# Kernel optimization log

Measured on AMD Instinct MI355X. Metric: run time of the kernel, lower is better.

## Reference

```python
import jax, jax.numpy as jnp
import numpy as np

DIM = 2048
HEADS = 16
B = 2
T = 2048


def setup_inputs() -> dict:
    key = jax.random.key(0)
    k_x, k_qkv, k_out, k_b = jax.random.split(key, 4)
    inv = DIM ** -0.5
    return {
        "x": jax.random.normal(k_x, (B, T, DIM), dtype=jnp.float32),
        "w_qkv": jax.random.normal(k_qkv, (DIM, 3 * DIM), dtype=jnp.float32) * inv,
        "w_out": jax.random.normal(k_out, (DIM, DIM), dtype=jnp.float32) * inv,
        "b_out": jnp.zeros((DIM,), dtype=jnp.float32),
    }


def reference(x, w_qkv, w_out, b_out):
    b, t, e = x.shape
    h = HEADS
    d = e // h
    scale = d ** -0.5
    qkv = x @ w_qkv                              # [b, t, 3e]
    q, k, v = jnp.split(qkv, 3, axis=-1)
    # [b, t, e] -> [b, h, t, d]
    q, k, v = (a.reshape(b, t, h, d).transpose(0, 2, 1, 3) for a in (q, k, v))
    dots = jnp.einsum("bhid,bhjd->bhij", q, k) * scale  # [b, h, t, t]
    causal_mask = jnp.triu(jnp.ones((t, t), dtype=bool), k=1)  # True where j > i
    dots = jnp.where(causal_mask[None, None, :, :], -jnp.inf, dots)
    attn = jax.nn.softmax(dots, axis=-1)
    out = jnp.einsum("bhij,bhjd->bhid", attn, v)  # [b, h, t, d]
    out = out.transpose(0, 2, 1, 3).reshape(b, t, e)
    return out @ w_out + b_out
```

## Files before the change

### kernel.cpp

```cpp
#include <hip/hip_runtime.h>
#include <stdint.h>

#define BATCH 2
#define TDIM 2048
#define EDIM 2048
#define NH 16
#define HD 128
#define E3 6144
#define MROWS 4096

typedef short v8bf __attribute__((ext_vector_type(8)));
typedef float v4f  __attribute__((ext_vector_type(4)));

typedef __attribute__((address_space(3))) uint8_t lds_u8;
typedef __attribute__((address_space(1))) uint8_t glb_u8;

__device__ __forceinline__ void gload16(const void* g, void* l) {
    __builtin_amdgcn_global_load_lds((const glb_u8*)g, (lds_u8*)l, 16, 0, 0);
}

__device__ __forceinline__ ushort f2bf(float f) {
    uint32_t u = __float_as_uint(f);
    return (ushort)((u + 0x7fffu + ((u >> 16) & 1u)) >> 16);
}

__global__ void cvtx_kernel(const float* __restrict__ in, ushort* __restrict__ out, int n) {
    int i = (blockIdx.x * 256 + threadIdx.x) * 4;
    const int stride = gridDim.x * 256 * 4;
    for (; i < n; i += stride) {
        const float4 v = *reinterpret_cast<const float4*>(in + i);
        ushort4 o = make_ushort4(f2bf(v.x), f2bf(v.y), f2bf(v.z), f2bf(v.w));
        *reinterpret_cast<ushort4*>(out + i) = o;
    }
}

__global__ void tcvt_kernel(const float* __restrict__ in, ushort* __restrict__ out, int R, int C) {
    __shared__ float t[32][33];
    const int tc = blockIdx.x * 32;
    const int tr = blockIdx.y * 32;
    const int tid = threadIdx.x;
    const int row = tid >> 3, c4 = (tid & 7) * 4;
    const float4 v = *reinterpret_cast<const float4*>(in + (size_t)(tr + row) * C + tc + c4);
    t[row][c4] = v.x; t[row][c4 + 1] = v.y; t[row][c4 + 2] = v.z; t[row][c4 + 3] = v.w;
    __syncthreads();
    const int oc = tid >> 3, r4 = (tid & 7) * 4;
    ushort4 o = make_ushort4(f2bf(t[r4][oc]), f2bf(t[r4 + 1][oc]),
                             f2bf(t[r4 + 2][oc]), f2bf(t[r4 + 3][oc]));
    *reinterpret_cast<ushort4*>(out + (size_t)(tc + oc) * R + tr + r4) = o;
}

__global__ void vtrans_kernel(const ushort* __restrict__ qkv, ushort* __restrict__ vt) {
    __shared__ ushort t[32][33];
    const int bh = blockIdx.z;
    const int b = bh >> 4, h = bh & 15;
    const int tr = blockIdx.x * 32;
    const int tc = blockIdx.y * 32;
    const int tid = threadIdx.x;
    const int row = tid >> 3, c4 = (tid & 7) * 4;
    const ushort4 v = *reinterpret_cast<const ushort4*>(
        qkv + (size_t)(b * TDIM + tr + row) * E3 + 2 * EDIM + h * HD + tc + c4);
    t[row][c4] = v.x; t[row][c4 + 1] = v.y; t[row][c4 + 2] = v.z; t[row][c4 + 3] = v.w;
    __syncthreads();
    const int oc = tid >> 3, r4 = (tid & 7) * 4;
    ushort4 o = make_ushort4(t[r4][oc], t[r4 + 1][oc], t[r4 + 2][oc], t[r4 + 3][oc]);
    *reinterpret_cast<ushort4*>(vt + (size_t)(bh * HD + tc + oc) * TDIM + tr + r4) = o;
}

__global__ __launch_bounds__(512, 2) void gemm256_kernel(const ushort* __restrict__ A,
                                                         const ushort* __restrict__ Bt,
                                                         ushort* __restrict__ C,
                                                         int Mdim, int Ndim, int Kdim) {
    __shared__ __align__(16) ushort Al[2][256 * 64];
    __shared__ __align__(16) ushort Bl[2][256 * 64];
    const int tid = threadIdx.x;
    const int lane = tid & 63;
    const int wv = tid >> 6;
    const int l4 = lane >> 4, l16 = lane & 15;
    const int wr = wv >> 2, wc = wv & 3;
    const int nbn = Ndim >> 8;
    const int nwg = (Mdim >> 8) * nbn;
    int bid = blockIdx.x;
    bid = (bid & 7) * (nwg >> 3) + (bid >> 3);
    const int bm = bid / nbn, bn = bid % nbn;

    const ushort* Abase = A + (size_t)(bm * 256) * Kdim;
    const ushort* Bbase = Bt + (size_t)(bn * 256) * Kdim;
    const int NT = Kdim >> 6;

    v4f acc[8][4] = {};

#define STAGE256(BUF, KT)                                                                     \
    do {                                                                                      \
        _Pragma("unroll") for (int i = 0; i < 4; ++i) {                                       \
            const int c = i * 512 + tid;                                                      \
            const int row = c >> 3;                                                           \
            const int kc = (c & 7) ^ (row & 7);                                               \
            gload16(Abase + (size_t)row * Kdim + (KT) * 64 + kc * 8,                          \
                    &Al[BUF][(i * 512 + wv * 64) * 8]);                                       \
        }                                                                                     \
        _Pragma("unroll") for (int i = 0; i < 4; ++i) {                                       \
            const int c = i * 512 + tid;                                                      \
            const int row = c >> 3;                                                           \
            const int kc = (c & 7) ^ (row & 7);                                               \
            gload16(Bbase + (size_t)row * Kdim + (KT) * 64 + kc * 8,                          \
                    &Bl[BUF][(i * 512 + wv * 64) * 8]);                                       \
        }                                                                                     \
    } while (0)

    STAGE256(0, 0);
    STAGE256(1, 1);
    asm volatile("s_waitcnt vmcnt(8)" ::: "memory");
    __builtin_amdgcn_s_barrier();
    asm volatile("" ::: "memory");

    int cur = 0;
    for (int t = 0; t < NT; ++t) {
        const ushort* As = &Al[cur][0];
        const ushort* Bs = &Bl[cur][0];
#pragma unroll
        for (int mh = 0; mh < 2; ++mh) {
            v8bf af[4][2];
#pragma unroll
            for (int m = 0; m < 4; ++m)
#pragma unroll
                for (int kk = 0; kk < 2; ++kk) {
                    const int r = wr * 128 + mh * 64 + m * 16 + l16;
                    const int slot = (kk * 4 + l4) ^ (l16 & 7);
                    af[m][kk] = *reinterpret_cast<const v8bf*>(&As[r * 64 + slot * 8]);
                }
#pragma unroll
            for (int nh = 0; nh < 2; ++nh) {
                v8bf bfr[2][2];
#pragma unroll
                for (int n = 0; n < 2; ++n)
#pragma unroll
                    for (int kk = 0; kk < 2; ++kk) {
                        const int r = wc * 64 + nh * 32 + n * 16 + l16;
                        const int slot = (kk * 4 + l4) ^ (l16 & 7);
                        bfr[n][kk] = *reinterpret_cast<const v8bf*>(&Bs[r * 64 + slot * 8]);
                    }
                __builtin_amdgcn_s_setprio(1);
#pragma unroll
                for (int kk = 0; kk < 2; ++kk)
#pragma unroll
                    for (int m = 0; m < 4; ++m)
#pragma unroll
                        for (int n = 0; n < 2; ++n)
                            acc[mh * 4 + m][nh * 2 + n] = __builtin_amdgcn_mfma_f32_16x16x32_bf16(
                                af[m][kk], bfr[n][kk], acc[mh * 4 + m][nh * 2 + n], 0, 0, 0);
                __builtin_amdgcn_s_setprio(0);
            }
        }
        if (t == NT - 1) break;

        __builtin_amdgcn_sched_barrier(0);
        __builtin_amdgcn_s_barrier();
        asm volatile("" ::: "memory");
        if (t + 2 < NT) {
            STAGE256(cur, t + 2);
            asm volatile("s_waitcnt vmcnt(8)" ::: "memory");
        } else {
            asm volatile("s_waitcnt vmcnt(0)" ::: "memory");
        }
        __builtin_amdgcn_s_barrier();
        asm volatile("" ::: "memory");
        __builtin_amdgcn_sched_barrier(0);
        cur ^= 1;
    }
#undef STAGE256

    const int r0 = bm * 256 + wr * 128 + l4 * 4;
    const int c0 = bn * 256 + wc * 64 + l16;
#pragma unroll
    for (int mi = 0; mi < 8; ++mi)
#pragma unroll
        for (int ni = 0; ni < 4; ++ni)
#pragma unroll
            for (int j = 0; j < 4; ++j)
                C[(size_t)(r0 + mi * 16 + j) * Ndim + c0 + ni * 16] = f2bf(acc[mi][ni][j]);
}

template <int OUTF32>
__global__ void gemm_kernel(const ushort* __restrict__ A, const ushort* __restrict__ Bt,
                            void* __restrict__ Cv, const float* __restrict__ bias,
                            int Mdim, int Ndim, int Kdim) {
    __shared__ __align__(16) ushort As[128 * 64];
    __shared__ __align__(16) ushort Bs[128 * 64];
    const int tid = threadIdx.x;
    const int lane = tid & 63;
    const int wv = tid >> 6;
    const int l4 = lane >> 4, l16 = lane & 15;
    const int nbn = Ndim >> 7;
    const int nwg = (Mdim >> 7) * nbn;
    int bid = blockIdx.x;
    bid = (bid & 7) * (nwg >> 3) + (bid >> 3);
    const int bm = bid / nbn, bn = bid % nbn;
    const int wr = wv >> 1, wc = wv & 1;

    const ushort* Abase = A + (size_t)(bm * 128) * Kdim;
    const ushort* Bbase = Bt + (size_t)(bn * 128) * Kdim;

    v4f acc[4][4] = {};

    for (int k0 = 0; k0 < Kdim; k0 += 64) {
#pragma unroll
        for (int i = 0; i < 4; ++i) {
            const int c = i * 256 + tid;
            const int row = c >> 3;
            const int kc = (c & 7) ^ (row & 7);
            gload16(Abase + (size_t)row * Kdim + k0 + kc * 8, &As[(i * 256 + wv * 64) * 8]);
        }
#pragma unroll
        for (int i = 0; i < 4; ++i) {
            const int c = i * 256 + tid;
            const int row = c >> 3;
            const int kc = (c & 7) ^ (row & 7);
            gload16(Bbase + (size_t)row * Kdim + k0 + kc * 8, &Bs[(i * 256 + wv * 64) * 8]);
        }
        __syncthreads();
#pragma unroll
        for (int kk = 0; kk < 2; ++kk) {
            v8bf af[4], bfr[4];
#pragma unroll
            for (int m = 0; m < 4; ++m) {
                const int r = wr * 64 + m * 16 + l16;
                const int slot = (kk * 4 + l4) ^ (r & 7);
                af[m] = *reinterpret_cast<const v8bf*>(&As[r * 64 + slot * 8]);
            }
#pragma unroll
            for (int n = 0; n < 4; ++n) {
                const int r = wc * 64 + n * 16 + l16;
                const int slot = (kk * 4 + l4) ^ (r & 7);
                bfr[n] = *reinterpret_cast<const v8bf*>(&Bs[r * 64 + slot * 8]);
            }
#pragma unroll
            for (int m = 0; m < 4; ++m)
#pragma unroll
                for (int n = 0; n < 4; ++n)
                    acc[m][n] = __builtin_amdgcn_mfma_f32_16x16x32_bf16(af[m], bfr[n], acc[m][n], 0, 0, 0);
        }
        __syncthreads();
    }

    const int r0 = bm * 128 + wr * 64 + l4 * 4;
    const int c0 = bn * 128 + wc * 64 + l16;
    if (OUTF32) {
        float* Cf = (float*)Cv;
#pragma unroll
        for (int n = 0; n < 4; ++n) {
            const float bv = bias[c0 + n * 16];
#pragma unroll
            for (int m = 0; m < 4; ++m)
#pragma unroll
                for (int j = 0; j < 4; ++j)
                    Cf[(size_t)(r0 + m * 16 + j) * Ndim + c0 + n * 16] = acc[m][n][j] + bv;
        }
    } else {
        ushort* Cb = (ushort*)Cv;
#pragma unroll
        for (int n = 0; n < 4; ++n)
#pragma unroll
            for (int m = 0; m < 4; ++m)
#pragma unroll
                for (int j = 0; j < 4; ++j)
                    Cb[(size_t)(r0 + m * 16 + j) * Ndim + c0 + n * 16] = f2bf(acc[m][n][j]);
    }
}

__global__ __launch_bounds__(256, 2) void flash_kernel(const ushort* __restrict__ qkv,
                                                       const ushort* __restrict__ vt,
                                                       ushort* __restrict__ ao) {
    __shared__ __align__(16) ushort Kl[2][64 * 128];
    __shared__ __align__(16) ushort Vl[2][128 * 64];
    __shared__ __align__(16) ushort Pl[128 * 64];

    const int xi = blockIdx.x;
    const int ti = (xi & 1) ? (xi >> 1) : (15 - (xi >> 1));
    const int h = blockIdx.y;
    const int b = blockIdx.z;
    const int tid = threadIdx.x;
    const int lane = tid & 63;
    const int wv = tid >> 6;
    const int l4 = lane >> 4, l16 = lane & 15;

    const int rbs[2]  = {ti * 64 + wv * 16, TDIM - 64 * (ti + 1) + wv * 16};
    const int diag[2] = {ti, 31 - ti};
    const int nkt = 32 - ti;

    v8bf qf[2][4];
#pragma unroll
    for (int mg = 0; mg < 2; ++mg) {
        const ushort* qp = qkv + (size_t)(b * TDIM + rbs[mg] + l16) * E3 + h * HD + l4 * 8;
#pragma unroll
        for (int d0 = 0; d0 < 4; ++d0) {
            v8bf r = *reinterpret_cast<const v8bf*>(qp + d0 * 32);
            v8bf o;
#pragma unroll
            for (int e = 0; e < 8; ++e) {
                const float f = __uint_as_float(((uint32_t)(ushort)r[e]) << 16) * 0.08838834764831845f;
                o[e] = (short)f2bf(f);
            }
            qf[mg][d0] = o;
        }
    }

    float mrun[2][4], lrun[2][4];
#pragma unroll
    for (int mg = 0; mg < 2; ++mg)
#pragma unroll
        for (int j = 0; j < 4; ++j) { mrun[mg][j] = -1e30f; lrun[mg][j] = 0.0f; }
    v4f oacc[2][8] = {};

    const ushort* kbase = qkv + (size_t)(b * TDIM) * E3 + EDIM + h * HD;
    const ushort* vbase = vt + (size_t)((b * 16 + h) * HD) * TDIM;

#define STAGE(BUF, KT)                                                                        \
    do {                                                                                      \
        _Pragma("unroll") for (int i = 0; i < 4; ++i) {                                       \
            const int c = i * 256 + tid;                                                      \
            const int row = c >> 4;                                                           \
            const int dc = (c & 15) ^ (row & 7);                                              \
            gload16(kbase + (size_t)((KT) * 64 + row) * E3 + dc * 8,                          \
                    &Kl[BUF][(i * 256 + wv * 64) * 8]);                                       \
        }                                                                                     \
        _Pragma("unroll") for (int i = 0; i < 4; ++i) {                                       \
            const int c = i * 256 + tid;                                                      \
            const int row = c >> 3;                                                           \
            const int jc = (c & 7) ^ (row & 7);                                               \
            gload16(vbase + (size_t)row * TDIM + (KT) * 64 + jc * 8,                          \
                    &Vl[BUF][(i * 256 + wv * 64) * 8]);                                       \
        }                                                                                     \
    } while (0)

    STAGE(0, 0);
    __syncthreads();
    int cur = 0;

    for (int kt = 0; kt < nkt; ++kt) {
        if (kt + 1 < nkt) STAGE(cur ^ 1, kt + 1);

        const bool act0 = (kt <= diag[0]);
        const ushort* Kb = &Kl[cur][0];
        const ushort* Vb = &Vl[cur][0];

        v4f s[2][4] = {};
#pragma unroll
        for (int d0 = 0; d0 < 4; ++d0) {
            v8bf kf[4];
#pragma unroll
            for (int kvn = 0; kvn < 4; ++kvn) {
                const int r = kvn * 16 + l16;
                const int slot = (d0 * 4 + l4) ^ (r & 7);
                kf[kvn] = *reinterpret_cast<const v8bf*>(&Kb[r * 128 + slot * 8]);
            }
#pragma unroll
            for (int kvn = 0; kvn < 4; ++kvn) {
                if (act0)
                    s[0][kvn] = __builtin_amdgcn_mfma_f32_16x16x32_bf16(qf[0][d0], kf[kvn], s[0][kvn], 0, 0, 0);
                s[1][kvn] = __builtin_amdgcn_mfma_f32_16x16x32_bf16(qf[1][d0], kf[kvn], s[1][kvn], 0, 0, 0);
            }
        }

#pragma unroll
        for (int mg = 0; mg < 2; ++mg) {
            if (mg == 0 && !act0) continue;

            float sv[4][4];
#pragma unroll
            for (int kvn = 0; kvn < 4; ++kvn)
#pragma unroll
                for (int j = 0; j < 4; ++j)
                    sv[kvn][j] = s[mg][kvn][j];

            if (kt == diag[mg]) {
                const int rg = rbs[mg] + l4 * 4;
#pragma unroll
                for (int kvn = 0; kvn < 4; ++kvn) {
                    const int cg = kt * 64 + kvn * 16 + l16;
#pragma unroll
                    for (int j = 0; j < 4; ++j)
                        if (cg > rg + j) sv[kvn][j] = -__builtin_inff();
                }
            }

            float pm[4], dmax = -1e30f;
#pragma unroll
            for (int j = 0; j < 4; ++j) {
                float m0 = fmaxf(fmaxf(sv[0][j], sv[1][j]), fmaxf(sv[2][j], sv[3][j]));
                m0 = fmaxf(m0, __shfl_xor(m0, 1));
                m0 = fmaxf(m0, __shfl_xor(m0, 2));
                m0 = fmaxf(m0, __shfl_xor(m0, 4));
                m0 = fmaxf(m0, __shfl_xor(m0, 8));
                pm[j] = m0;
                dmax = fmaxf(dmax, m0 - mrun[mg][j]);
            }
            if (!__all(dmax <= 8.0f)) {
                float corr[4];
#pragma unroll
                for (int j = 0; j < 4; ++j) {
                    const float mn = fmaxf(mrun[mg][j], pm[j]);
                    corr[j] = __expf(mrun[mg][j] - mn);
                    mrun[mg][j] = mn;
                    lrun[mg][j] *= corr[j];
                }
#pragma unroll
                for (int n = 0; n < 8; ++n)
#pragma unroll
                    for (int j = 0; j < 4; ++j)
                        oacc[mg][n][j] *= corr[j];
            }

            float p[4][4];
#pragma unroll
            for (int kvn = 0; kvn < 4; ++kvn)
#pragma unroll
                for (int j = 0; j < 4; ++j)
                    p[kvn][j] = __expf(sv[kvn][j] - mrun[mg][j]);
#pragma unroll
            for (int j = 0; j < 4; ++j)
                lrun[mg][j] += p[0][j] + p[1][j] + p[2][j] + p[3][j];

            const int row = wv * 32 + mg * 16 + l4 * 4;
#pragma unroll
            for (int kvn = 0; kvn < 4; ++kvn) {
                const int cc = kvn * 2 + (l16 >> 3);
#pragma unroll
                for (int j = 0; j < 4; ++j) {
                    const int r = row + j;
                    Pl[r * 64 + ((cc ^ (r & 7)) * 8) + (l16 & 7)] = f2bf(p[kvn][j]);
                }
            }
        }

#pragma unroll
        for (int kk = 0; kk < 2; ++kk) {
            v8bf pf[2];
#pragma unroll
            for (int mg = 0; mg < 2; ++mg) {
                if (mg == 0 && !act0) continue;
                const int r = wv * 32 + mg * 16 + l16;
                const int slot = (kk * 4 + l4) ^ (r & 7);
                pf[mg] = *reinterpret_cast<const v8bf*>(&Pl[r * 64 + slot * 8]);
            }
#pragma unroll
            for (int n = 0; n < 8; ++n) {
                const int dr = n * 16 + l16;
                const int slot = (kk * 4 + l4) ^ (dr & 7);
                v8bf vf = *reinterpret_cast<const v8bf*>(&Vb[dr * 64 + slot * 8]);
                if (act0)
                    oacc[0][n] = __builtin_amdgcn_mfma_f32_16x16x32_bf16(pf[0], vf, oacc[0][n], 0, 0, 0);
                oacc[1][n] = __builtin_amdgcn_mfma_f32_16x16x32_bf16(pf[1], vf, oacc[1][n], 0, 0, 0);
            }
        }
        __syncthreads();
        cur ^= 1;
    }
#undef STAGE

#pragma unroll
    for (int mg = 0; mg < 2; ++mg) {
        float inv[4];
#pragma unroll
        for (int j = 0; j < 4; ++j) {
            float l = lrun[mg][j];
            l += __shfl_xor(l, 1);
            l += __shfl_xor(l, 2);
            l += __shfl_xor(l, 4);
            l += __shfl_xor(l, 8);
            inv[j] = 1.0f / l;
        }
        ushort* aop = ao + (size_t)(b * TDIM + rbs[mg] + l4 * 4) * EDIM + h * HD + l16;
#pragma unroll
        for (int n = 0; n < 8; ++n)
#pragma unroll
            for (int j = 0; j < 4; ++j)
                aop[(size_t)j * EDIM + n * 16] = f2bf(oacc[mg][n][j] * inv[j]);
    }
}

extern "C" void kernel_launch(void* const* d_in, const int* in_sizes, int n_in,
                              void* d_out, int out_size, void* d_ws, size_t ws_size,
                              hipStream_t stream) {
    (void)in_sizes; (void)n_in; (void)out_size; (void)ws_size;
    const float* x     = (const float*)d_in[0];
    const float* w_qkv = (const float*)d_in[1];
    const float* w_out = (const float*)d_in[2];
    const float* b_out = (const float*)d_in[3];

    uint8_t* ws = (uint8_t*)d_ws;
    ushort* qkv   = (ushort*)(ws);
    ushort* woutT = (ushort*)(ws + 50331648u);
    ushort* xb    = (ushort*)(ws + 58720256u);
    ushort* wqkvT = (ushort*)(ws + 75497472u);
    ushort* vtb   = xb;
    ushort* ao    = wqkvT;

    cvtx_kernel<<<2048, 256, 0, stream>>>(x, xb, MROWS * EDIM);
    tcvt_kernel<<<dim3(E3 / 32, EDIM / 32), 256, 0, stream>>>(w_qkv, wqkvT, EDIM, E3);
    tcvt_kernel<<<dim3(EDIM / 32, EDIM / 32), 256, 0, stream>>>(w_out, woutT, EDIM, EDIM);

    gemm256_kernel<<<(MROWS / 256) * (E3 / 256), 512, 0, stream>>>(
        xb, wqkvT, qkv, MROWS, E3, EDIM);

    vtrans_kernel<<<dim3(TDIM / 32, HD / 32, BATCH * NH), 256, 0, stream>>>(qkv, vtb);

    flash_kernel<<<dim3(16, NH, BATCH), 256, 0, stream>>>(qkv, vtb, ao);

    gemm_kernel<1><<<(MROWS / 128) * (EDIM / 128), 256, 0, stream>>>(
        ao, woutT, d_out, b_out, MROWS, EDIM, EDIM);
}
```

Measured before the change: 289.0 us.

## Restructure QKV GEMM into 128x256 tiles with split-phase staged loads

Replaces the 256x256-tile QKV projection GEMM with a 128x256-tile kernel. Each K step is split into two halves, and global-to-LDS loads for upcoming tiles are interleaved between the MFMA phases behind extra barriers. The aim is to overlap memory traffic with compute more finely, cut LDS and register footprint per block, and double the number of workgroups for better CU occupancy. In exchange, each block reuses its B tile over fewer rows, and each K step carries more barriers.

Result: faster. 276.7 us (-4.3%).

```diff
diff --git a/kernel.cpp b/kernel.cpp
--- a/kernel.cpp
+++ b/kernel.cpp
@@ -66,118 +66,137 @@
     *reinterpret_cast<ushort4*>(vt + (size_t)(bh * HD + tc + oc) * TDIM + tr + r4) = o;
 }
 
-__global__ __launch_bounds__(512, 2) void gemm256_kernel(const ushort* __restrict__ A,
-                                                         const ushort* __restrict__ Bt,
-                                                         ushort* __restrict__ C,
-                                                         int Mdim, int Ndim, int Kdim) {
-    __shared__ __align__(16) ushort Al[2][256 * 64];
-    __shared__ __align__(16) ushort Bl[2][256 * 64];
+__global__ __launch_bounds__(512, 2) void gemm8p_kernel(const ushort* __restrict__ A,
+                                                        const ushort* __restrict__ Bt,
+                                                        ushort* __restrict__ C,
+                                                        int Mdim, int Ndim, int Kdim) {
+    __shared__ __align__(16) ushort AL[2][128 * 64];
+    __shared__ __align__(16) ushort BL[2][256 * 64];
     const int tid = threadIdx.x;
     const int lane = tid & 63;
     const int wv = tid >> 6;
     const int l4 = lane >> 4, l16 = lane & 15;
     const int wr = wv >> 2, wc = wv & 3;
     const int nbn = Ndim >> 8;
-    const int nwg = (Mdim >> 8) * nbn;
+    const int nwg = (Mdim >> 7) * nbn;
     int bid = blockIdx.x;
     bid = (bid & 7) * (nwg >> 3) + (bid >> 3);
     const int bm = bid / nbn, bn = bid % nbn;
 
-    const ushort* Abase = A + (size_t)(bm * 256) * Kdim;
+    const ushort* Abase = A + (size_t)(bm * 128) * Kdim;
     const ushort* Bbase = Bt + (size_t)(bn * 256) * Kdim;
     const int NT = Kdim >> 6;
 
-    v4f acc[8][4] = {};
-
-#define STAGE256(BUF, KT)                                                                     \
-    do {                                                                                      \
-        _Pragma("unroll") for (int i = 0; i < 4; ++i) {                                       \
-            const int c = i * 512 + tid;                                                      \
-            const int row = c >> 3;                                                           \
-            const int kc = (c & 7) ^ (row & 7);                                               \
-            gload16(Abase + (size_t)row * Kdim + (KT) * 64 + kc * 8,                          \
-                    &Al[BUF][(i * 512 + wv * 64) * 8]);                                       \
-        }                                                                                     \
-        _Pragma("unroll") for (int i = 0; i < 4; ++i) {                                       \
-            const int c = i * 512 + tid;                                                      \
-            const int row = c >> 3;                                                           \
-            const int kc = (c & 7) ^ (row & 7);                                               \
-            gload16(Bbase + (size_t)row * Kdim + (KT) * 64 + kc * 8,                          \
-                    &Bl[BUF][(i * 512 + wv * 64) * 8]);                                       \
-        }                                                                                     \
+    const int arow = tid >> 3;
+    const int akc = (tid & 7) ^ (arow & 7);
+
+#define STAGE_A(BUF, T, H)                                                                   \
+    gload16(Abase + (size_t)((H) * 64 + arow) * Kdim + (T) * 64 + akc * 8,                   \
+            &AL[BUF][((H) * 512 + wv * 64) * 8])
+#define STAGE_B(BUF, T, H)                                                                   \
+    do {                                                                                     \
+        gload16(Bbase + (size_t)((H) * 128 + arow) * Kdim + (T) * 64 + akc * 8,              \
+                &BL[BUF][((H) * 1024 + wv * 64) * 8]);                                       \
+        gload16(Bbase + (size_t)((H) * 128 + 64 + arow) * Kdim + (T) * 64 + akc * 8,         \
+                &BL[BUF][((H) * 1024 + 512 + wv * 64) * 8]);                                 \
     } while (0)
 
-    STAGE256(0, 0);
-    STAGE256(1, 1);
-    asm volatile("s_waitcnt vmcnt(8)" ::: "memory");
+    STAGE_A(0, 0, 0); STAGE_A(0, 0, 1); STAGE_B(0, 0, 0); STAGE_B(0, 0, 1);
+    STAGE_A(1, 1, 0); STAGE_B(1, 1, 0); STAGE_B(1, 1, 1);
+    asm volatile("s_waitcnt vmcnt(5)" ::: "memory");
     __builtin_amdgcn_s_barrier();
-    asm volatile("" ::: "memory");
-
-    int cur = 0;
+
+    v4f acc[2][2][2][2] = {};
+
     for (int t = 0; t < NT; ++t) {
-        const ushort* As = &Al[cur][0];
-        const ushort* Bs = &Bl[cur][0];
-#pragma unroll
-        for (int mh = 0; mh < 2; ++mh) {
-            v8bf af[4][2];
-#pragma unroll
-            for (int m = 0; m < 4; ++m)
+        const int cur = t & 1;
+        const ushort* As = &AL[cur][0];
+        const ushort* Bs = &BL[cur][0];
+        v8bf af[2][2], bfr[2][2][2];
+
+#pragma unroll
+        for (int m = 0; m < 2; ++m)
+#pragma unroll
+            for (int kk = 0; kk < 2; ++kk) {
+                const int rA = wr * 32 + m * 16 + l16;
+                const int slot = (kk * 4 + l4) ^ (l16 & 7);
+                af[m][kk] = *reinterpret_cast<const v8bf*>(&As[rA * 64 + slot * 8]);
+            }
+#pragma unroll
+        for (int nh = 0; nh < 2; ++nh)
+#pragma unroll
+            for (int n = 0; n < 2; ++n)
 #pragma unroll
                 for (int kk = 0; kk < 2; ++kk) {
-                    const int r = wr * 128 + mh * 64 + m * 16 + l16;
+                    const int rB = nh * 128 + wc * 32 + n * 16 + l16;
                     const int slot = (kk * 4 + l4) ^ (l16 & 7);
-                    af[m][kk] = *reinterpret_cast<const v8bf*>(&As[r * 64 + slot * 8]);
+                    bfr[nh][n][kk] = *reinterpret_cast<const v8bf*>(&Bs[rB * 64 + slot * 8]);
                 }
-#pragma unroll
-            for (int nh = 0; nh < 2; ++nh) {
-                v8bf bfr[2][2];
-#pragma unroll
-                for (int n = 0; n < 2; ++n)
-#pragma unroll
-                    for (int kk = 0; kk < 2; ++kk) {
-                        const int r = wc * 64 + nh * 32 + n * 16 + l16;
-                        const int slot = (kk * 4 + l4) ^ (l16 & 7);
-                        bfr[n][kk] = *reinterpret_cast<const v8bf*>(&Bs[r * 64 + slot * 8]);
-                    }
-                __builtin_amdgcn_s_setprio(1);
-#pragma unroll
-                for (int kk = 0; kk < 2; ++kk)
-#pragma unroll
-                    for (int m = 0; m < 4; ++m)
-#pragma unroll
-                        for (int n = 0; n < 2; ++n)
-                            acc[mh * 4 + m][nh * 2 + n] = __builtin_amdgcn_mfma_f32_16x16x32_bf16(
-                                af[m][kk], bfr[n][kk], acc[mh * 4 + m][nh * 2 + n], 0, 0, 0);
-                __builtin_amdgcn_s_setprio(0);
-            }
-        }
-        if (t == NT - 1) break;
-
-        __builtin_amdgcn_sched_barrier(0);
+        if (t + 1 < NT) STAGE_A(cur ^ 1, t + 1, 1);
         __builtin_amdgcn_s_barrier();
-        asm volatile("" ::: "memory");
+        __builtin_amdgcn_s_setprio(1);
+#pragma unroll
+        for (int kk = 0; kk < 2; ++kk)
+#pragma unroll
+            for (int m = 0; m < 2; ++m)
+#pragma unroll
+                for (int nh = 0; nh < 2; ++nh)
+#pragma unroll
+                    for (int n = 0; n < 2; ++n)
+                        acc[0][nh][m][n] = __builtin_amdgcn_mfma_f32_16x16x32_bf16(
+                            af[m][kk], bfr[nh][n][kk], acc[0][nh][m][n], 0, 0, 0);
+        __builtin_amdgcn_s_setprio(0);
+        __builtin_amdgcn_s_barrier();
+
+#pragma unroll
+        for (int m = 0; m < 2; ++m)
+#pragma unroll
+            for (int kk = 0; kk < 2; ++kk) {
+                const int rA = 64 + wr * 32 + m * 16 + l16;
+                const int slot = (kk * 4 + l4) ^ (l16 & 7);
+                af[m][kk] = *reinterpret_cast<const v8bf*>(&As[rA * 64 + slot * 8]);
+            }
         if (t + 2 < NT) {
-            STAGE256(cur, t + 2);
-            asm volatile("s_waitcnt vmcnt(8)" ::: "memory");
-        } else {
+            STAGE_A(cur, t + 2, 0);
+            STAGE_B(cur, t + 2, 0);
+            STAGE_B(cur, t + 2, 1);
+        }
+        __builtin_amdgcn_s_barrier();
+        __builtin_amdgcn_s_setprio(1);
+#pragma unroll
+        for (int kk = 0; kk < 2; ++kk)
+#pragma unroll
+            for (int m = 0; m < 2; ++m)
+#pragma unroll
+                for (int nh = 0; nh < 2; ++nh)
+#pragma unroll
+                    for (int n = 0; n < 2; ++n)
+                        acc[1][nh][m][n] = __builtin_amdgcn_mfma_f32_16x16x32_bf16(
+                            af[m][kk], bfr[nh][n][kk], acc[1][nh][m][n], 0, 0, 0);
+        __builtin_amdgcn_s_setprio(0);
+        if (t + 2 < NT)
+            asm volatile("s_waitcnt vmcnt(5)" ::: "memory");
+        else if (t + 1 < NT)
             asm volatile("s_waitcnt vmcnt(0)" ::: "memory");
-        }
         __builtin_amdgcn_s_barrier();
-        asm volatile("" ::: "memory");
-        __builtin_amdgcn_sched_barrier(0);
-        cur ^= 1;
-    }
-#undef STAGE256
-
-    const int r0 = bm * 256 + wr * 128 + l4 * 4;
-    const int c0 = bn * 256 + wc * 64 + l16;
-#pragma unroll
-    for (int mi = 0; mi < 8; ++mi)
-#pragma unroll
-        for (int ni = 0; ni < 4; ++ni)
-#pragma unroll
-            for (int j = 0; j < 4; ++j)
-                C[(size_t)(r0 + mi * 16 + j) * Ndim + c0 + ni * 16] = f2bf(acc[mi][ni][j]);
+    }
+#undef STAGE_A
+#undef STAGE_B
+
+#pragma unroll
+    for (int mh = 0; mh < 2; ++mh)
+#pragma unroll
+        for (int m = 0; m < 2; ++m)
+#pragma unroll
+            for (int nh = 0; nh < 2; ++nh)
+#pragma unroll
+                for (int n = 0; n < 2; ++n) {
+                    const int r0 = bm * 128 + mh * 64 + wr * 32 + m * 16 + l4 * 4;
+                    const int c0 = bn * 256 + nh * 128 + wc * 32 + n * 16 + l16;
+#pragma unroll
+                    for (int j = 0; j < 4; ++j)
+                        C[(size_t)(r0 + j) * Ndim + c0] = f2bf(acc[mh][nh][m][n][j]);
+                }
 }
 
 template <int OUTF32>
@@ -499,7 +518,7 @@
     tcvt_kernel<<<dim3(E3 / 32, EDIM / 32), 256, 0, stream>>>(w_qkv, wqkvT, EDIM, E3);
     tcvt_kernel<<<dim3(EDIM / 32, EDIM / 32), 256, 0, stream>>>(w_out, woutT, EDIM, EDIM);
 
-    gemm256_kernel<<<(MROWS / 256) * (E3 / 256), 512, 0, stream>>>(
+    gemm8p_kernel<<<(MROWS / 128) * (E3 / 256), 512, 0, stream>>>(
         xb, wqkvT, qkv, MROWS, E3, EDIM);
 
     vtrans_kernel<<<dim3(TDIM / 32, HD / 32, BATCH * NH), 256, 0, stream>>>(qkv, vtb);
```
